# Optimization experiments

Hardware: AMD Instinct MI355X
Metric: run time of the kernel (lower is better)

## Reference

```python
import jax, jax.numpy as jnp
import numpy as np

B, H, W, C = 8, 32, 32, 384
NH, HD = 6, 64
SCALE = HD ** -0.5


def setup_inputs() -> dict:
    key = jax.random.key(0)
    ks = jax.random.split(key, 7)
    return {
        "x": jax.random.normal(ks[0], (B, H, W, C), jnp.float32),
        "qkv_w": jax.random.normal(ks[1], (C, 3 * C), jnp.float32) * 0.02,
        "qkv_b": jax.random.normal(ks[2], (3 * C,), jnp.float32) * 0.02,
        "proj_w": jax.random.normal(ks[3], (C, C), jnp.float32) * 0.02,
        "proj_b": jax.random.normal(ks[4], (C,), jnp.float32) * 0.02,
        "rel_pos_h": jax.random.normal(ks[5], (2 * H - 1, HD), jnp.float32) * 0.02,
        "rel_pos_w": jax.random.normal(ks[6], (2 * W - 1, HD), jnp.float32) * 0.02,
    }


def _get_rel_pos(rel_pos, q_size, k_size):
    # q_size == k_size and rel_pos already has 2*size-1 rows -> interpolation is identity
    coords = jnp.arange(q_size)[:, None] - jnp.arange(k_size)[None, :] + (k_size - 1)
    return rel_pos[coords]  # [q, k, head_dim]


def reference(x, qkv_w, qkv_b, proj_w, proj_b, rel_pos_h, rel_pos_w):
    b, h, w, c = x.shape
    hw = h * w
    qkv = x.reshape(b, hw, c) @ qkv_w + qkv_b            # [B, HW, 3C]
    qkv = qkv.reshape(b, hw, 3, NH, HD).transpose(2, 0, 3, 1, 4)
    qkv = qkv.reshape(3, b * NH, hw, HD)
    q, k, v = qkv[0], qkv[1], qkv[2]                      # [B*nH, HW, hd]

    attn = jnp.einsum('bqd,bkd->bqk', q * SCALE, k)       # [B*nH, HW, HW]

    Rh = _get_rel_pos(rel_pos_h, h, h)                    # [H, H, hd]
    Rw = _get_rel_pos(rel_pos_w, w, w)                    # [W, W, hd]
    r_q = q.reshape(b * NH, h, w, HD)
    rel_h = jnp.einsum('bhwc,hkc->bhwk', r_q, Rh)         # [B*nH, H, W, kH]
    rel_w = jnp.einsum('bhwc,wkc->bhwk', r_q, Rw)         # [B*nH, H, W, kW]
    attn = attn.reshape(b * NH, h, w, h, w) + rel_h[:, :, :, :, None] + rel_w[:, :, :, None, :]
    attn = attn.reshape(b * NH, hw, hw)

    attn = jax.nn.softmax(attn, axis=-1)
    out = jnp.einsum('bqk,bkd->bqd', attn, v)             # [B*nH, HW, hd]
    out = out.reshape(b, NH, h, w, HD).transpose(0, 2, 3, 1, 4).reshape(b, h, w, c)
    return out @ proj_w + proj_b
```

## Files before the change

### kernel.cpp

```cpp
#include <hip/hip_runtime.h>

typedef __attribute__((ext_vector_type(8))) short bf16x8;
typedef __attribute__((ext_vector_type(4))) float f32x4;

#define MFMA(a, b, c) __builtin_amdgcn_mfma_f32_16x16x32_bf16((a), (b), (c), 0, 0, 0)
#define LOG2E 1.4426950408889634f

__device__ __forceinline__ unsigned short f2bf(float f) {
    union { float f; unsigned u; } v; v.f = f;
    unsigned r = v.u + 0x7FFFu + ((v.u >> 16) & 1u);
    return (unsigned short)(r >> 16);
}
__device__ __forceinline__ float bf2f(unsigned short h) {
    union { unsigned u; float f; } v; v.u = ((unsigned)h) << 16;
    return v.f;
}
__device__ __forceinline__ float exp2fast(float x) {
#if __has_builtin(__builtin_amdgcn_exp2f)
    return __builtin_amdgcn_exp2f(x);
#else
    float r; asm("v_exp_f32 %0, %1" : "=v"(r) : "v"(x)); return r;
#endif
}
__device__ __forceinline__ void gload16(const void* g, void* l) {
    __builtin_amdgcn_global_load_lds(
        (const __attribute__((address_space(1))) void*)g,
        (__attribute__((address_space(3))) void*)l, 16, 0, 0);
}

#define WS_QHI   0
#define WS_QLO   6291456
#define WS_KHI   12582912
#define WS_KLO   18874368
#define WS_VTHI  25165824
#define WS_RELH  37748736
#define WS_RELW  40894464
#define WS_WTH   44040192
#define WS_WTL   44924928
#define WS_PWTH  45809664
#define WS_PWTL  46104576
#define WS_XHI   46399488
#define WS_XLO   52690944

__global__ __launch_bounds__(256) void prep_fused(const float* __restrict__ x,
        const float* __restrict__ qkv_w, const float* __restrict__ proj_w,
        unsigned short* __restrict__ xh,
        unsigned short* __restrict__ wth, unsigned short* __restrict__ pwth) {
    __shared__ float tile[64][65];
    const int bid = blockIdx.x;
    const int t = threadIdx.x;
    if (bid < 3072) {
        int i = bid * 256 + t;
        float4 v = ((const float4*)x)[i];
        float f[4] = {v.x, v.y, v.z, v.w};
#pragma unroll
        for (int j = 0; j < 4; ++j)
            xh[i * 4 + j] = f2bf(f[j]);
        return;
    }
    const float* w; unsigned short *oh; int K, N, bx, by;
    if (bid < 3180) {
        int b2 = bid - 3072;
        w = qkv_w; oh = wth; K = 384; N = 1152;
        bx = b2 % 18; by = b2 / 18;
    } else {
        int b3 = bid - 3180;
        w = proj_w; oh = pwth; K = 384; N = 384;
        bx = b3 % 6; by = b3 / 6;
    }
    const int k0 = by * 64, n0 = bx * 64;
#pragma unroll
    for (int i = 0; i < 16; ++i) {
        int idx = t + i * 256;
        int r = idx >> 6, c = idx & 63;
        tile[r][c] = w[(size_t)(k0 + r) * N + n0 + c];
    }
    __syncthreads();
#pragma unroll
    for (int i = 0; i < 16; ++i) {
        int idx = t + i * 256;
        int r = idx >> 6, c = idx & 63;
        oh[(size_t)(n0 + r) * K + k0 + c] = f2bf(tile[c][r]);
    }
}

__global__ __launch_bounds__(256) void qkv_gemm_mfma(
        const unsigned short* __restrict__ xh,
        const unsigned short* __restrict__ wth,
        const float* __restrict__ bias,
        unsigned short* __restrict__ qh,
        unsigned short* __restrict__ kh,
        unsigned short* __restrict__ vth) {
    __shared__ unsigned short Ah[2][4096], Bh[2][4096];
    const int t = threadIdx.x;
    const int lane = t & 63, wid = t >> 6;
    const int C = lane & 15, G = lane >> 4;
    const int nbid = (blockIdx.x & 7) * 288 + (blockIdx.x >> 3);
    const int row0 = (nbid / 18) * 64, col0 = (nbid % 18) * 64;
    const int rl = wid * 16 + (lane >> 3);
    const int cbyt = ((lane & 7) << 4) ^ ((lane >> 3) << 4);
    const char* pAh = (const char*)xh + (size_t)(row0 + rl) * 768 + cbyt;
    const char* pBh = (const char*)wth + (size_t)(col0 + rl) * 768 + cbyt;
    const int dof = wid * 2048;
    gload16(pAh, (char*)Ah[0] + dof); gload16(pAh + 6144, (char*)Ah[0] + dof + 1024);
    gload16(pBh, (char*)Bh[0] + dof); gload16(pBh + 6144, (char*)Bh[0] + dof + 1024);
    int cur = 0;
    f32x4 acc[4] = {};
    for (int kb = 0; kb < 6; ++kb) {
        if (kb < 5) {
            const int o = (kb + 1) * 128;
            gload16(pAh + o, (char*)Ah[cur^1] + dof); gload16(pAh + o + 6144, (char*)Ah[cur^1] + dof + 1024);
            gload16(pBh + o, (char*)Bh[cur^1] + dof); gload16(pBh + o + 6144, (char*)Bh[cur^1] + dof + 1024);
            __builtin_amdgcn_sched_barrier(0);
            asm volatile("s_waitcnt vmcnt(4)" ::: "memory");
        } else {
            asm volatile("s_waitcnt vmcnt(0)" ::: "memory");
        }
        __builtin_amdgcn_s_barrier();
        __builtin_amdgcn_sched_barrier(0);
        const unsigned short* AhB = Ah[cur];
        const unsigned short* BhB = Bh[cur];
#pragma unroll
        for (int ks = 0; ks < 2; ++ks) {
            int arow = wid * 16 + C;
            int aoff = arow * 128 + ((ks * 64 + G * 16) ^ ((arow & 7) << 4));
            bf16x8 ah = *(const bf16x8*)((char*)AhB + aoff);
#pragma unroll
            for (int s = 0; s < 4; ++s) {
                int brow = s * 16 + C;
                int boff = brow * 128 + ((ks * 64 + G * 16) ^ ((brow & 7) << 4));
                bf16x8 bh = *(const bf16x8*)((char*)BhB + boff);
                acc[s] = MFMA(ah, bh, acc[s]);
            }
        }
        __builtin_amdgcn_s_barrier();
        cur ^= 1;
    }
#pragma unroll
    for (int s = 0; s < 4; ++s) {
        int n = col0 + s * 16 + C;
        float bv = bias[n];
        int tsel = n / 384;
        int rem = n - tsel * 384;
        int head = rem >> 6, d = rem & 63;
#pragma unroll
        for (int r = 0; r < 4; ++r) {
            int m = row0 + wid * 16 + 4 * G + r;
            int b = m >> 10, hw = m & 1023;
            int g = b * 6 + head;
            float val = acc[s][r] + bv;
            if (tsel == 0) val *= 0.125f * LOG2E;
            unsigned short h = f2bf(val);
            if (tsel == 2) {
                vth[((size_t)g * 64 + d) * 1024 + hw] = h;
            } else {
                size_t o = ((size_t)g * 1024 + hw) * 64 + d;
                if (tsel == 0) qh[o] = h;
                else           kh[o] = h;
            }
        }
    }
}

__global__ __launch_bounds__(256) void rel_mfma(
        const unsigned short* __restrict__ qh,
        const float* __restrict__ rph, const float* __restrict__ rpw,
        unsigned short* __restrict__ relh, unsigned short* __restrict__ relw) {
    __shared__ unsigned short Bs[32 * 64];
    const int t = threadIdx.x;
    const int lane = t & 63, wid = t >> 6;
    const int C = lane & 15, G = lane >> 4;
    const int pos = blockIdx.x;
    const int g0 = blockIdx.y * 8;
    const int mode = blockIdx.z;
    const float* rp = (mode == 0) ? rph : rpw;
    {
        int k = t >> 3, d8 = t & 7;
        const float* src = rp + (size_t)(pos + 31 - k) * 64 + d8 * 8;
        float4 f0 = *(const float4*)src;
        float4 f1 = *(const float4*)(src + 4);
        unsigned short hv[8] = { f2bf(f0.x), f2bf(f0.y), f2bf(f0.z), f2bf(f0.w),
                                 f2bf(f1.x), f2bf(f1.y), f2bf(f1.z), f2bf(f1.w) };
        int bo = k * 128 + ((d8 * 16) ^ ((k & 7) << 4));
        *(bf16x8*)((char*)Bs + bo) = *(bf16x8*)hv;
    }
    __syncthreads();
    bf16x8 bf[2][2];
#pragma unroll
    for (int s = 0; s < 2; ++s)
#pragma unroll
        for (int ks = 0; ks < 2; ++ks) {
            int row = s * 16 + C;
            int off = row * 128 + ((ks * 64 + G * 16) ^ ((row & 7) << 4));
            bf[s][ks] = *(const bf16x8*)((char*)Bs + off);
        }
#pragma unroll
    for (int ib = 0; ib < 4; ++ib) {
        int arow = ib * 64 + wid * 16 + C;
        int gi = arow >> 5, w = arow & 31;
        int hw = (mode == 0) ? (pos * 32 + w) : (w * 32 + pos);
        const unsigned short* qrow = qh + ((size_t)(g0 + gi) * 1024 + hw) * 64;
        bf16x8 a0 = *(const bf16x8*)(qrow + G * 8);
        bf16x8 a1 = *(const bf16x8*)(qrow + 32 + G * 8);
        f32x4 acc[2] = {};
#pragma unroll
        for (int s = 0; s < 2; ++s) {
            acc[s] = MFMA(a0, bf[s][0], acc[s]);
            acc[s] = MFMA(a1, bf[s][1], acc[s]);
        }
        unsigned short* dst = (mode == 0) ? relh : relw;
#pragma unroll
        for (int s = 0; s < 2; ++s)
#pragma unroll
            for (int rr = 0; rr < 4; ++rr) {
                int orow = ib * 64 + wid * 16 + 4 * G + rr;
                int ogi = orow >> 5, ow = orow & 31;
                int ohw = (mode == 0) ? (pos * 32 + ow) : (ow * 32 + pos);
                dst[((size_t)(g0 + ogi) * 1024 + ohw) * 32 + s * 16 + C] =
                    f2bf(acc[s][rr] * 8.0f);
            }
    }
}

__global__ __launch_bounds__(256) void attn_mfma(
        const unsigned short* __restrict__ qh,
        const unsigned short* __restrict__ kh_g,
        const unsigned short* __restrict__ vth_g,
        const unsigned short* __restrict__ relh, const unsigned short* __restrict__ relw,
        unsigned short* __restrict__ atth) {
    __shared__ unsigned short Kh[2][4096], Vh[2][4096];
    __shared__ unsigned short Pl[4][1024];
    __shared__ unsigned short RelU[4][16 * 34];
    const int t = threadIdx.x;
    const int lane = t & 63, wid = t >> 6;
    const int C = lane & 15, G = lane >> 4;
    const int bid = blockIdx.x;
    const int wgid = (bid & 7) * 96 + (bid >> 3);
    const int g = wgid >> 4, qb = wgid & 15;
    const int qtile = qb * 64 + wid * 16;

    {
        const unsigned short* src = relh + ((size_t)g * 1024 + qb * 64) * 32;
#pragma unroll
        for (int j = 0; j < 8; ++j) {
            int i = t + j * 256;
            int row = i >> 5, col = i & 31;
            RelU[row >> 4][(row & 15) * 34 + col] = src[i];
        }
    }
    const int cbyt = ((lane & 7) << 4) ^ ((lane >> 3) << 4);
    const char* khbase = (const char*)(kh_g + (size_t)g * 65536)
                         + (wid * 16 + (lane >> 3)) * 128 + cbyt;
    const char* vhbase = (const char*)(vth_g + (size_t)g * 65536)
                         + (wid * 16 + (lane >> 3)) * 2048 + cbyt;
    bf16x8 qfh[2];
    {
        size_t qo = ((size_t)g * 1024 + qtile + C) * 64;
        qfh[0] = *(const bf16x8*)(qh + qo + G * 8);
        qfh[1] = *(const bf16x8*)(qh + qo + 32 + G * 8);
    }
    float rw8[2][4];
    {
        const unsigned short* rwp = relw + ((size_t)g * 1024 + qtile + C) * 32;
#pragma unroll
        for (int e = 0; e < 2; ++e)
#pragma unroll
            for (int r = 0; r < 4; ++r)
                rw8[e][r] = bf2f(rwp[e * 16 + 4 * G + r]);
    }
    f32x4 O[4] = {};
    float m_ = -1e30f, l_ = 0.f;
    unsigned short* Pw = Pl[wid];

    __syncthreads();
    {
        char* dK = (char*)Kh[0] + wid * 2048;
        char* dV = (char*)Vh[0] + wid * 2048;
        gload16(khbase, dK); gload16(khbase + 1024, dK + 1024);
        gload16(vhbase, dV); gload16(vhbase + 16384, dV + 1024);
    }
    int cur = 0;

    for (int kb = 0; kb < 16; ++kb) {
        if (kb < 15) {
            char* dK = (char*)Kh[cur ^ 1] + wid * 2048;
            char* dV = (char*)Vh[cur ^ 1] + wid * 2048;
            const char* sK = khbase + (kb + 1) * 8192;
            const char* sV = vhbase + (kb + 1) * 128;
            gload16(sK, dK); gload16(sK + 1024, dK + 1024);
            gload16(sV, dV); gload16(sV + 16384, dV + 1024);
            __builtin_amdgcn_sched_barrier(0);
            asm volatile("s_waitcnt vmcnt(4)" ::: "memory");
        } else {
            asm volatile("s_waitcnt vmcnt(0)" ::: "memory");
        }
        __builtin_amdgcn_s_barrier();
        __builtin_amdgcn_sched_barrier(0);
        const unsigned short* khbuf = Kh[cur];
        const unsigned short* vhbuf = Vh[cur];
        f32x4 S[4] = {};
        __builtin_amdgcn_s_setprio(1);
#pragma unroll
        for (int ks = 0; ks < 2; ++ks) {
#pragma unroll
            for (int s = 0; s < 4; ++s) {
                int row = s * 16 + C;
                int off = row * 128 + ((ks * 64 + G * 16) ^ ((row & 7) << 4));
                bf16x8 bh = *(const bf16x8*)((char*)khbuf + off);
                S[s] = MFMA(bh, qfh[ks], S[s]);
            }
        }
        __builtin_amdgcn_s_setprio(0);
        {
            unsigned rp = *(const unsigned*)((const char*)&RelU[wid][0]
                                             + C * 68 + 4 * kb);
            float rh0 = bf2f((unsigned short)(rp & 0xFFFF));
            float rh1 = bf2f((unsigned short)(rp >> 16));
#pragma unroll
            for (int s = 0; s < 4; ++s) {
                float rh = (s < 2) ? rh0 : rh1;
#pragma unroll
                for (int r = 0; r < 4; ++r)
                    S[s][r] += rh + rw8[s & 1][r];
            }
        }
        float mt = fmaxf(fmaxf(fmaxf(S[0][0], S[0][1]), fmaxf(S[0][2], S[0][3])),
                         fmaxf(fmaxf(S[1][0], S[1][1]), fmaxf(S[1][2], S[1][3])));
        mt = fmaxf(mt, fmaxf(fmaxf(fmaxf(S[2][0], S[2][1]), fmaxf(S[2][2], S[2][3])),
                             fmaxf(fmaxf(S[3][0], S[3][1]), fmaxf(S[3][2], S[3][3]))));
        mt = fmaxf(mt, __shfl_xor(mt, 16));
        mt = fmaxf(mt, __shfl_xor(mt, 32));
        if (__any(mt - m_ > 11.f)) {
            float mn = fmaxf(m_, mt);
            float corr = exp2fast(m_ - mn);
            m_ = mn;
            l_ *= corr;
            float cO[4];
#pragma unroll
            for (int r = 0; r < 4; ++r) cO[r] = __shfl(corr, 4 * G + r);
#pragma unroll
            for (int s = 0; s < 4; ++s)
#pragma unroll
                for (int r = 0; r < 4; ++r) O[s][r] *= cO[r];
        }
        float lt = 0.f;
#pragma unroll
        for (int s = 0; s < 4; ++s)
#pragma unroll
            for (int r = 0; r < 4; ++r) {
                S[s][r] = exp2fast(S[s][r] - m_);
                lt += S[s][r];
            }
        l_ += lt;
#pragma unroll
        for (int s = 0; s < 4; ++s) {
            unsigned d0, d1;
            asm("v_cvt_pk_bf16_f32 %0, %1, %2" : "=v"(d0) : "v"(S[s][0]), "v"(S[s][1]));
            asm("v_cvt_pk_bf16_f32 %0, %1, %2" : "=v"(d1) : "v"(S[s][2]), "v"(S[s][3]));
            int bo = C * 128 + (((s * 16 + 4 * G) * 2) ^ ((C & 7) << 4));
            uint2 dv; dv.x = d0; dv.y = d1;
            *(uint2*)((char*)Pw + bo) = dv;
        }
        __builtin_amdgcn_s_setprio(1);
#pragma unroll
        for (int ks = 0; ks < 2; ++ks) {
            int aoff = C * 128 + ((ks * 64 + G * 16) ^ ((C & 7) << 4));
            bf16x8 pa = *(const bf16x8*)((char*)Pw + aoff);
#pragma unroll
            for (int s = 0; s < 4; ++s) {
                int vrow = s * 16 + C;
                int voff = vrow * 128 + ((ks * 64 + G * 16) ^ ((vrow & 7) << 4));
                bf16x8 vh = *(const bf16x8*)((char*)vhbuf + voff);
                O[s] = MFMA(pa, vh, O[s]);
            }
        }
        __builtin_amdgcn_s_setprio(0);
        __builtin_amdgcn_s_barrier();
        cur ^= 1;
    }
    l_ += __shfl_xor(l_, 16);
    l_ += __shfl_xor(l_, 32);
    const int b = g / 6, head = g - b * 6;
#pragma unroll
    for (int r = 0; r < 4; ++r) {
        float inv = 1.0f / __shfl(l_, 4 * G + r);
        int token = qtile + 4 * G + r;
        size_t ob = ((size_t)b * 1024 + token) * 384 + head * 64;
#pragma unroll
        for (int s = 0; s < 4; ++s)
            atth[ob + s * 16 + C] = f2bf(O[s][r] * inv);
    }
}

__global__ __launch_bounds__(256) void proj_gemm_mfma(
        const unsigned short* __restrict__ ah_g,
        const unsigned short* __restrict__ bth,
        const float* __restrict__ bias, float* __restrict__ out) {
    __shared__ unsigned short Ah[2][4096], Bh[2][4096];
    const int t = threadIdx.x;
    const int lane = t & 63, wid = t >> 6;
    const int C = lane & 15, G = lane >> 4;
    const int nbid = (blockIdx.x & 7) * 96 + (blockIdx.x >> 3);
    const int row0 = (nbid / 6) * 64, col0 = (nbid % 6) * 64;
    const int rl = wid * 16 + (lane >> 3);
    const int cbyt = ((lane & 7) << 4) ^ ((lane >> 3) << 4);
    const char* pAh = (const char*)ah_g + (size_t)(row0 + rl) * 768 + cbyt;
    const char* pBh = (const char*)bth + (size_t)(col0 + rl) * 768 + cbyt;
    const int dof = wid * 2048;
    gload16(pAh, (char*)Ah[0] + dof); gload16(pAh + 6144, (char*)Ah[0] + dof + 1024);
    gload16(pBh, (char*)Bh[0] + dof); gload16(pBh + 6144, (char*)Bh[0] + dof + 1024);
    int cur = 0;
    f32x4 acc[4] = {};
    for (int kb = 0; kb < 6; ++kb) {
        if (kb < 5) {
            const int o = (kb + 1) * 128;
            gload16(pAh + o, (char*)Ah[cur^1] + dof); gload16(pAh + o + 6144, (char*)Ah[cur^1] + dof + 1024);
            gload16(pBh + o, (char*)Bh[cur^1] + dof); gload16(pBh + o + 6144, (char*)Bh[cur^1] + dof + 1024);
            __builtin_amdgcn_sched_barrier(0);
            asm volatile("s_waitcnt vmcnt(4)" ::: "memory");
        } else {
            asm volatile("s_waitcnt vmcnt(0)" ::: "memory");
        }
        __builtin_amdgcn_s_barrier();
        __builtin_amdgcn_sched_barrier(0);
        const unsigned short* AhB = Ah[cur];
        const unsigned short* BhB = Bh[cur];
#pragma unroll
        for (int ks = 0; ks < 2; ++ks) {
            int arow = wid * 16 + C;
            int aoff = arow * 128 + ((ks * 64 + G * 16) ^ ((arow & 7) << 4));
            bf16x8 ah = *(const bf16x8*)((char*)AhB + aoff);
#pragma unroll
            for (int s = 0; s < 4; ++s) {
                int brow = s * 16 + C;
                int boff = brow * 128 + ((ks * 64 + G * 16) ^ ((brow & 7) << 4));
                bf16x8 bh = *(const bf16x8*)((char*)BhB + boff);
                acc[s] = MFMA(ah, bh, acc[s]);
            }
        }
        __builtin_amdgcn_s_barrier();
        cur ^= 1;
    }
#pragma unroll
    for (int s = 0; s < 4; ++s) {
        int n = col0 + s * 16 + C;
        float bv = bias[n];
#pragma unroll
        for (int r = 0; r < 4; ++r) {
            int m = row0 + wid * 16 + 4 * G + r;
            out[(size_t)m * 384 + n] = acc[s][r] + bv;
        }
    }
}

extern "C" void kernel_launch(void* const* d_in, const int* in_sizes, int n_in,
                              void* d_out, int out_size, void* d_ws, size_t ws_size,
                              hipStream_t stream) {
    const float* x      = (const float*)d_in[0];
    const float* qkv_w  = (const float*)d_in[1];
    const float* qkv_b  = (const float*)d_in[2];
    const float* proj_w = (const float*)d_in[3];
    const float* proj_b = (const float*)d_in[4];
    const float* rph    = (const float*)d_in[5];
    const float* rpw    = (const float*)d_in[6];
    char* ws = (char*)d_ws;

    unsigned short* QHI  = (unsigned short*)(ws + WS_QHI);
    unsigned short* KHI  = (unsigned short*)(ws + WS_KHI);
    unsigned short* VTHI = (unsigned short*)(ws + WS_VTHI);
    unsigned short* RELH = (unsigned short*)(ws + WS_RELH);
    unsigned short* RELW = (unsigned short*)(ws + WS_RELW);
    unsigned short* WTH  = (unsigned short*)(ws + WS_WTH);
    unsigned short* PWTH = (unsigned short*)(ws + WS_PWTH);
    unsigned short* XHI  = (unsigned short*)(ws + WS_XHI);
    unsigned short* ATTH = XHI;

    prep_fused<<<3216, 256, 0, stream>>>(x, qkv_w, proj_w, XHI, WTH, PWTH);
    qkv_gemm_mfma<<<2304, 256, 0, stream>>>(XHI, WTH, qkv_b, QHI, KHI, VTHI);
    rel_mfma<<<dim3(32, 6, 2), 256, 0, stream>>>(QHI, rph, rpw, RELH, RELW);
    attn_mfma<<<768, 256, 0, stream>>>(QHI, KHI, VTHI, RELH, RELW, ATTH);
    proj_gemm_mfma<<<768, 256, 0, stream>>>(ATTH, PWTH, proj_b, (float*)d_out);
}
```

Baseline: 78.47 us.

## Triple-buffer K tiles in attention, vectorize bf16 stores, use 3-input max

The attention kernel now prefetches K tiles two iterations ahead using a third LDS buffer, while V stays double-buffered. The vmcnt waits are adjusted to match the larger number of loads in flight. The prep and QKV GEMM epilogues pack bf16 values into 64-bit stores: for x conversion, and for the transposed V output, whose four rows are contiguous along hw. The row-max reduction is restructured into three-operand fmax calls so the compiler can emit v_max3, and the extra LDS buffer slightly raises shared memory use per block.

```diff
diff --git a/kernel.cpp b/kernel.cpp
--- a/kernel.cpp
+++ b/kernel.cpp
@@ -21,6 +21,9 @@
 #else
     float r; asm("v_exp_f32 %0, %1" : "=v"(r) : "v"(x)); return r;
 #endif
+}
+__device__ __forceinline__ float fm3(float a, float b, float c) {
+    return fmaxf(fmaxf(a, b), c);
 }
 __device__ __forceinline__ void gload16(const void* g, void* l) {
     __builtin_amdgcn_global_load_lds(
@@ -52,10 +55,10 @@
     if (bid < 3072) {
         int i = bid * 256 + t;
         float4 v = ((const float4*)x)[i];
-        float f[4] = {v.x, v.y, v.z, v.w};
-#pragma unroll
-        for (int j = 0; j < 4; ++j)
-            xh[i * 4 + j] = f2bf(f[j]);
+        uint2 o;
+        o.x = (unsigned)f2bf(v.x) | ((unsigned)f2bf(v.y) << 16);
+        o.y = (unsigned)f2bf(v.z) | ((unsigned)f2bf(v.w) << 16);
+        *(uint2*)&xh[i * 4] = o;
         return;
     }
     const float* w; unsigned short *oh; int K, N, bx, by;
@@ -143,20 +146,25 @@
         int tsel = n / 384;
         int rem = n - tsel * 384;
         int head = rem >> 6, d = rem & 63;
-#pragma unroll
-        for (int r = 0; r < 4; ++r) {
-            int m = row0 + wid * 16 + 4 * G + r;
-            int b = m >> 10, hw = m & 1023;
-            int g = b * 6 + head;
-            float val = acc[s][r] + bv;
-            if (tsel == 0) val *= 0.125f * LOG2E;
-            unsigned short h = f2bf(val);
-            if (tsel == 2) {
-                vth[((size_t)g * 64 + d) * 1024 + hw] = h;
-            } else {
-                size_t o = ((size_t)g * 1024 + hw) * 64 + d;
-                if (tsel == 0) qh[o] = h;
-                else           kh[o] = h;
+        int m0 = row0 + wid * 16 + 4 * G;
+        int b = m0 >> 10, hw0 = m0 & 1023;
+        int g = b * 6 + head;
+        if (tsel == 2) {
+            unsigned short hv[4];
+#pragma unroll
+            for (int r = 0; r < 4; ++r) hv[r] = f2bf(acc[s][r] + bv);
+            uint2 pv;
+            pv.x = (unsigned)hv[0] | ((unsigned)hv[1] << 16);
+            pv.y = (unsigned)hv[2] | ((unsigned)hv[3] << 16);
+            *(uint2*)&vth[((size_t)g * 64 + d) * 1024 + hw0] = pv;
+        } else {
+#pragma unroll
+            for (int r = 0; r < 4; ++r) {
+                float val = acc[s][r] + bv;
+                if (tsel == 0) val *= 0.125f * LOG2E;
+                size_t o = ((size_t)g * 1024 + hw0 + r) * 64 + d;
+                if (tsel == 0) qh[o] = f2bf(val);
+                else           kh[o] = f2bf(val);
             }
         }
     }
@@ -228,7 +236,7 @@
         const unsigned short* __restrict__ vth_g,
         const unsigned short* __restrict__ relh, const unsigned short* __restrict__ relw,
         unsigned short* __restrict__ atth) {
-    __shared__ unsigned short Kh[2][4096], Vh[2][4096];
+    __shared__ unsigned short Kh[3][4096], Vh[2][4096];
     __shared__ unsigned short Pl[4][1024];
     __shared__ unsigned short RelU[4][16 * 34];
     const int t = threadIdx.x;
@@ -274,30 +282,33 @@
 
     __syncthreads();
     {
-        char* dK = (char*)Kh[0] + wid * 2048;
-        char* dV = (char*)Vh[0] + wid * 2048;
-        gload16(khbase, dK); gload16(khbase + 1024, dK + 1024);
-        gload16(vhbase, dV); gload16(vhbase + 16384, dV + 1024);
-    }
-    int cur = 0;
+        char* dK0 = (char*)Kh[0] + wid * 2048;
+        char* dV0 = (char*)Vh[0] + wid * 2048;
+        char* dK1 = (char*)Kh[1] + wid * 2048;
+        gload16(khbase, dK0);          gload16(khbase + 1024, dK0 + 1024);
+        gload16(vhbase, dV0);          gload16(vhbase + 16384, dV0 + 1024);
+        gload16(khbase + 8192, dK1);   gload16(khbase + 9216, dK1 + 1024);
+    }
 
     for (int kb = 0; kb < 16; ++kb) {
         if (kb < 15) {
-            char* dK = (char*)Kh[cur ^ 1] + wid * 2048;
-            char* dV = (char*)Vh[cur ^ 1] + wid * 2048;
-            const char* sK = khbase + (kb + 1) * 8192;
             const char* sV = vhbase + (kb + 1) * 128;
+            char* dV = (char*)Vh[(kb + 1) & 1] + wid * 2048;
+            gload16(sV, dV); gload16(sV + 16384, dV + 1024);
+        }
+        if (kb < 14) {
+            const char* sK = khbase + (kb + 2) * 8192;
+            char* dK = (char*)Kh[(kb + 2) % 3] + wid * 2048;
             gload16(sK, dK); gload16(sK + 1024, dK + 1024);
-            gload16(sV, dV); gload16(sV + 16384, dV + 1024);
-            __builtin_amdgcn_sched_barrier(0);
-            asm volatile("s_waitcnt vmcnt(4)" ::: "memory");
-        } else {
-            asm volatile("s_waitcnt vmcnt(0)" ::: "memory");
-        }
-        __builtin_amdgcn_s_barrier();
+        }
         __builtin_amdgcn_sched_barrier(0);
-        const unsigned short* khbuf = Kh[cur];
-        const unsigned short* vhbuf = Vh[cur];
+        if (kb < 14)      { asm volatile("s_waitcnt vmcnt(6)" ::: "memory"); }
+        else if (kb < 15) { asm volatile("s_waitcnt vmcnt(4)" ::: "memory"); }
+        else              { asm volatile("s_waitcnt vmcnt(0)" ::: "memory"); }
+        __builtin_amdgcn_s_barrier();
+        __builtin_amdgcn_sched_barrier(0);
+        const unsigned short* khbuf = Kh[kb % 3];
+        const unsigned short* vhbuf = Vh[kb & 1];
         f32x4 S[4] = {};
         __builtin_amdgcn_s_setprio(1);
 #pragma unroll
@@ -324,10 +335,12 @@
                     S[s][r] += rh + rw8[s & 1][r];
             }
         }
-        float mt = fmaxf(fmaxf(fmaxf(S[0][0], S[0][1]), fmaxf(S[0][2], S[0][3])),
-                         fmaxf(fmaxf(S[1][0], S[1][1]), fmaxf(S[1][2], S[1][3])));
-        mt = fmaxf(mt, fmaxf(fmaxf(fmaxf(S[2][0], S[2][1]), fmaxf(S[2][2], S[2][3])),
-                             fmaxf(fmaxf(S[3][0], S[3][1]), fmaxf(S[3][2], S[3][3]))));
+        float mt = fm3(fm3(fm3(S[0][0], S[0][1], S[0][2]),
+                           fm3(S[0][3], S[1][0], S[1][1]),
+                           fm3(S[1][2], S[1][3], S[2][0])),
+                       fm3(S[2][1], S[2][2], S[2][3]),
+                       fm3(S[3][0], S[3][1], S[3][2]));
+        mt = fmaxf(mt, S[3][3]);
         mt = fmaxf(mt, __shfl_xor(mt, 16));
         mt = fmaxf(mt, __shfl_xor(mt, 32));
         if (__any(mt - m_ > 11.f)) {
@@ -376,7 +389,6 @@
         }
         __builtin_amdgcn_s_setprio(0);
         __builtin_amdgcn_s_barrier();
-        cur ^= 1;
     }
     l_ += __shfl_xor(l_, 16);
     l_ += __shfl_xor(l_, 32);
```

Result: faster. 71.75 us, median of 3 (-8.6%).
